# Optimization experiments

Measured on AMD Instinct MI355X. Metric: run time of the kernel, lower is better.

The kernel has to match this reference:

```python
import jax, jax.numpy as jnp
import numpy as np

D = 512      # d_model
H = 8        # n_heads
HD = D // H  # head_dim = 64
PS = 4       # patch_size
B, T, P = 4, 4096, 1024


def setup_inputs() -> dict:
    key = jax.random.key(0)
    ks = jax.random.split(key, 12)
    s = 1.0 / np.sqrt(D)
    return {
        "token_hidden": jax.random.normal(ks[0], (B, T, D), jnp.float32),
        "patch_hidden": jax.random.normal(ks[1], (B, P, D), jnp.float32),
        "Wq": jax.random.normal(ks[2], (D, D), jnp.float32) * s,
        "Wk": jax.random.normal(ks[3], (D, D), jnp.float32) * s,
        "Wv": jax.random.normal(ks[4], (D, D), jnp.float32) * s,
        "bq": jax.random.normal(ks[5], (D,), jnp.float32) * 0.02,
        "bk": jax.random.normal(ks[6], (D,), jnp.float32) * 0.02,
        "bv": jax.random.normal(ks[7], (D,), jnp.float32) * 0.02,
        "Wo": jax.random.normal(ks[8], (D, D), jnp.float32) * s,
        "bo": jax.random.normal(ks[9], (D,), jnp.float32) * 0.02,
    }


def reference(token_hidden, patch_hidden, Wq, Wk, Wv, bq, bk, bv, Wo, bo):
    b, t, _ = token_hidden.shape
    p = patch_hidden.shape[1]
    # QKV projections (equivalent to nn.MultiheadAttention in_proj)
    q = (token_hidden @ Wq + bq).reshape(b, t, H, HD)
    k = (patch_hidden @ Wk + bk).reshape(b, p, H, HD)
    v = (patch_hidden @ Wv + bv).reshape(b, p, H, HD)
    # scaled dot-product scores: [b, h, t, p]
    scores = jnp.einsum('bthd,bphd->bhtp', q, k) / jnp.sqrt(jnp.asarray(HD, q.dtype))
    # block-causal token-to-patch mask: token i attends to patches 0..i//PS
    allowed = jnp.arange(p)[None, :] <= (jnp.arange(t)[:, None] // PS)  # [t, p]
    scores = jnp.where(allowed[None, None, :, :], scores, -jnp.inf)
    attn = jax.nn.softmax(scores, axis=-1)
    ctx = jnp.einsum('bhtp,bphd->bthd', attn, v).reshape(b, t, D)
    out = ctx @ Wo + bo  # out_proj
    return token_hidden + out
```

## Files before the change

kernel.cpp:

```cpp
#include <hip/hip_runtime.h>
#include <stdint.h>

#define DM 512
#define NH 8
#define HDIM 64
#define TT 4096
#define PP 1024

typedef float f32x4 __attribute__((ext_vector_type(4)));
typedef __bf16 bf16x8 __attribute__((ext_vector_type(8)));
typedef unsigned short u16x8 __attribute__((ext_vector_type(8)));
typedef unsigned short u16x4 __attribute__((ext_vector_type(4)));
typedef unsigned int u32x2 __attribute__((ext_vector_type(2)));

static __device__ __forceinline__ unsigned short f2bf(float f) {
  unsigned u = __builtin_bit_cast(unsigned, f);
  u += 0x7fff + ((u >> 16) & 1);
  return (unsigned short)(u >> 16);
}

static __device__ __forceinline__ unsigned packbf(float a, float b) {
  unsigned ua = __builtin_bit_cast(unsigned, a) + 0x8000u;
  unsigned ub = __builtin_bit_cast(unsigned, b) + 0x8000u;
  return __builtin_amdgcn_perm(ub, ua, 0x07060302u);
}

static __device__ __forceinline__ void load_lds16(const void* g, void* l) {
  __builtin_amdgcn_global_load_lds(
      (__attribute__((address_space(1))) void*)g,
      (__attribute__((address_space(3))) void*)l, 16, 0, 0);
}

static __device__ __forceinline__ f32x4 mfma16(bf16x8 a, bf16x8 b, f32x4 c) {
  return __builtin_amdgcn_mfma_f32_16x16x32_bf16(a, b, c, 0, 0, 0);
}

__global__ __launch_bounds__(256) void k_convert(
    const float* __restrict__ tok, const float* __restrict__ pat,
    const float* __restrict__ wq, const float* __restrict__ wk,
    const float* __restrict__ wv, const float* __restrict__ wo,
    unsigned short* __restrict__ xtok, unsigned short* __restrict__ xpat,
    unsigned short* __restrict__ wt) {
  const int gid = blockIdx.x * 256 + threadIdx.x;
  const int NX = 2621440;
  if (gid < NX) {
    int i4 = gid * 4;
    const float* src;
    unsigned short* dst;
    int idx;
    if (i4 < 8388608) { src = tok; dst = xtok; idx = i4; }
    else              { src = pat; dst = xpat; idx = i4 - 8388608; }
    f32x4 v = *(const f32x4*)&src[idx];
    u16x4 o;
#pragma unroll
    for (int i = 0; i < 4; ++i) o[i] = f2bf(v[i]);
    *(u16x4*)&dst[idx] = o;
  } else {
    int wi = gid - NX;
    int wid = wi >> 16;
    int e = (wi & 65535) << 2;
    int k = e >> 9, n = e & 511;
    const float* w = (wid == 0) ? wq : (wid == 1) ? wk : (wid == 2) ? wv : wo;
    f32x4 v = *(const f32x4*)&w[e];
    unsigned short* wtb = wt + (wid << 18);
#pragma unroll
    for (int i = 0; i < 4; ++i) wtb[(n + i) * 512 + k] = f2bf(v[i]);
  }
}

__device__ __forceinline__ void gemm_body(
    const unsigned short* __restrict__ A, const unsigned short* __restrict__ Wt,
    const float* __restrict__ bias, unsigned short* __restrict__ outb,
    float* __restrict__ outf, const float* __restrict__ resid, int mode,
    int bid, unsigned short* sA, unsigned short* sB) {
  const int tid = threadIdx.x;
  const int wave = tid >> 6, lane = tid & 63;
  const int q = lane >> 4, c = lane & 15;
  const int bm = bid >> 2, bn = bid & 3;
  const int wm = (wave >> 1) * 64, wn = (wave & 1) * 64;
  const int lr = lane >> 2, lc = (lane & 3) * 8;

  f32x4 acc[4][4];
#pragma unroll
  for (int i = 0; i < 4; ++i)
#pragma unroll
    for (int j = 0; j < 4; ++j) acc[i][j] = (f32x4){0.f, 0.f, 0.f, 0.f};

  const int rowA0 = bm * 128, rowB0 = bn * 128;

  for (int k0 = 0; k0 < 512; k0 += 32) {
#pragma unroll
    for (int qq = 0; qq < 2; ++qq) {
      const int chunk = wave * 2 + qq;
      load_lds16(&A[(rowA0 + chunk * 16 + lr) * 512 + k0 + lc], &sA[chunk * 512]);
      load_lds16(&Wt[(rowB0 + chunk * 16 + lr) * 512 + k0 + lc], &sB[chunk * 512]);
    }
    __syncthreads();
    bf16x8 af[4], bfr[4];
#pragma unroll
    for (int mt = 0; mt < 4; ++mt)
      af[mt] = __builtin_bit_cast(bf16x8, *(const u16x8*)&sA[(wm + mt * 16 + c) * 32 + q * 8]);
#pragma unroll
    for (int nt = 0; nt < 4; ++nt)
      bfr[nt] = __builtin_bit_cast(bf16x8, *(const u16x8*)&sB[(wn + nt * 16 + c) * 32 + q * 8]);
#pragma unroll
    for (int mt = 0; mt < 4; ++mt)
#pragma unroll
      for (int nt = 0; nt < 4; ++nt)
        acc[mt][nt] = mfma16(af[mt], bfr[nt], acc[mt][nt]);
    __syncthreads();
  }

  const float vs = (mode == 0) ? 0.125f : 1.0f;
#pragma unroll
  for (int nt = 0; nt < 4; ++nt) {
    const int col = bn * 128 + wn + nt * 16 + c;
    const float bcol = bias[col];
#pragma unroll
    for (int mt = 0; mt < 4; ++mt) {
      const int row0 = bm * 128 + wm + mt * 16 + q * 4;
#pragma unroll
      for (int r = 0; r < 4; ++r) {
        const int row = row0 + r;
        const float v = (acc[mt][nt][r] + bcol) * vs;
        if (mode == 3) {
          const int o = row * 512 + col;
          outf[o] = v + resid[o];
        } else if (mode == 2) {
          outb[((row >> 10) << 19) + (col << 10) + (row & 1023)] = f2bf(v);
        } else {
          outb[row * 512 + col] = f2bf(v);
        }
      }
    }
  }
}

__global__ __launch_bounds__(256) void k_gemm(
    const unsigned short* __restrict__ A, const unsigned short* __restrict__ Wt,
    const float* __restrict__ bias, unsigned short* __restrict__ outb,
    float* __restrict__ outf, const float* __restrict__ resid, int mode) {
  __shared__ unsigned short sA[128 * 32];
  __shared__ unsigned short sB[128 * 32];
  gemm_body(A, Wt, bias, outb, outf, resid, mode, blockIdx.x, sA, sB);
}

__global__ __launch_bounds__(256) void k_gemm_kv(
    const unsigned short* __restrict__ A,
    const unsigned short* __restrict__ WtK, const unsigned short* __restrict__ WtV,
    const float* __restrict__ bk, const float* __restrict__ bv,
    unsigned short* __restrict__ KB, unsigned short* __restrict__ VTB) {
  __shared__ unsigned short sA[128 * 32];
  __shared__ unsigned short sB[128 * 32];
  const int kv = blockIdx.x >> 7;
  const int bid = blockIdx.x & 127;
  if (kv == 0)
    gemm_body(A, WtK, bk, KB, nullptr, nullptr, 1, bid, sA, sB);
  else
    gemm_body(A, WtV, bv, VTB, nullptr, nullptr, 2, bid, sA, sB);
}

__global__ __launch_bounds__(256) void k_attn(
    const unsigned short* __restrict__ Q,
    const unsigned short* __restrict__ K,
    const unsigned short* __restrict__ VT,
    unsigned short* __restrict__ CTX) {
  __shared__ unsigned short sK[32 * 80];
  __shared__ unsigned short sV[64 * 40];
  __shared__ unsigned short sPT[4 * 32 * 40];

  const int tid = threadIdx.x;
  const int lane = tid & 63;
  const int wave = tid >> 6;
  const int q = lane >> 4, c = lane & 15;

  const int i = blockIdx.x >> 5;
  const int tg = (i & 1) ? (31 - (i >> 1)) : (i >> 1);
  const int bh = blockIdx.x & 31;
  const int b = bh >> 3, h = bh & 7;
  const int t0 = tg * 128 + wave * 32;
  const int tA = t0 + c, tB = t0 + 16 + c;

  const int qbA = (b * TT + tA) * 512 + h * 64 + q * 8;
  const int qbB = (b * TT + tB) * 512 + h * 64 + q * 8;
  const bf16x8 qfA0 = __builtin_bit_cast(bf16x8, *(const u16x8*)&Q[qbA]);
  const bf16x8 qfA1 = __builtin_bit_cast(bf16x8, *(const u16x8*)&Q[qbA + 32]);
  const bf16x8 qfB0 = __builtin_bit_cast(bf16x8, *(const u16x8*)&Q[qbB]);
  const bf16x8 qfB1 = __builtin_bit_cast(bf16x8, *(const u16x8*)&Q[qbB + 32]);

  f32x4 oA[4], oB[4];
#pragma unroll
  for (int m = 0; m < 4; ++m) {
    oA[m] = (f32x4){0.f, 0.f, 0.f, 0.f};
    oB[m] = (f32x4){0.f, 0.f, 0.f, 0.f};
  }
  f32x4 lA = (f32x4){0.f, 0.f, 0.f, 0.f};
  f32x4 lB = lA;
  const u16x8 onesu = {0x3F80, 0x3F80, 0x3F80, 0x3F80, 0x3F80, 0x3F80, 0x3F80, 0x3F80};
  const bf16x8 ones = __builtin_bit_cast(bf16x8, onesu);

  const int ntile = tg + 1;
  const int krow = tid >> 3, kcol = (tid & 7) * 8;
  const int vrow = tid >> 2, vcol = (tid & 3) * 8;
  const int kg = (b * PP + krow) * 512 + h * 64 + kcol;
  const int vg = (b << 19) + ((h * 64 + vrow) << 10) + vcol;
  unsigned short* sp = &sPT[wave * 1280];

  for (int pt = 0; pt < ntile; ++pt) {
    const int p0 = pt * 32;
    const u16x8 kreg = *(const u16x8*)&K[kg + p0 * 512];
    const u16x8 vreg = *(const u16x8*)&VT[vg + p0];
    __syncthreads();
    *(u16x8*)&sK[krow * 80 + kcol] = kreg;
    *(u16x8*)&sV[vrow * 40 + vcol] = vreg;
    __syncthreads();

    const bf16x8 ka0 = __builtin_bit_cast(bf16x8, *(const u16x8*)&sK[c * 80 + q * 8]);
    const bf16x8 ka1 = __builtin_bit_cast(bf16x8, *(const u16x8*)&sK[c * 80 + 32 + q * 8]);
    const bf16x8 kb0 = __builtin_bit_cast(bf16x8, *(const u16x8*)&sK[(16 + c) * 80 + q * 8]);
    const bf16x8 kb1 = __builtin_bit_cast(bf16x8, *(const u16x8*)&sK[(16 + c) * 80 + 32 + q * 8]);

    const f32x4 z = (f32x4){0.f, 0.f, 0.f, 0.f};
    f32x4 sA0 = mfma16(ka1, qfA1, mfma16(ka0, qfA0, z));
    f32x4 sA1 = mfma16(kb1, qfA1, mfma16(kb0, qfA0, z));
    f32x4 sB0 = mfma16(ka1, qfB1, mfma16(ka0, qfB0, z));
    f32x4 sB1 = mfma16(kb1, qfB1, mfma16(kb0, qfB0, z));

    if (pt + 1 == ntile) {
      const int limA = tA >> 2, limB = tB >> 2;
      const int pb0 = p0 + q * 4, pb1 = p0 + 16 + q * 4;
#pragma unroll
      for (int r = 0; r < 4; ++r) {
        if (pb0 + r > limA) sA0[r] = -1e30f;
        if (pb1 + r > limA) sA1[r] = -1e30f;
        if (pb0 + r > limB) sB0[r] = -1e30f;
        if (pb1 + r > limB) sB1[r] = -1e30f;
      }
    }

    float pA0[4], pA1[4], pB0[4], pB1[4];
#pragma unroll
    for (int r = 0; r < 4; ++r) {
      pA0[r] = __expf(sA0[r]);
      pA1[r] = __expf(sA1[r]);
      pB0[r] = __expf(sB0[r]);
      pB1[r] = __expf(sB1[r]);
    }

    {
      u32x2 w;
      w[0] = packbf(pA0[0], pA0[1]); w[1] = packbf(pA0[2], pA0[3]);
      *(u32x2*)&sp[c * 40 + q * 4] = w;
      w[0] = packbf(pA1[0], pA1[1]); w[1] = packbf(pA1[2], pA1[3]);
      *(u32x2*)&sp[c * 40 + 16 + q * 4] = w;
      w[0] = packbf(pB0[0], pB0[1]); w[1] = packbf(pB0[2], pB0[3]);
      *(u32x2*)&sp[(16 + c) * 40 + q * 4] = w;
      w[0] = packbf(pB1[0], pB1[1]); w[1] = packbf(pB1[2], pB1[3]);
      *(u32x2*)&sp[(16 + c) * 40 + 16 + q * 4] = w;
    }
    const bf16x8 pbA = __builtin_bit_cast(bf16x8, *(const u16x8*)&sp[c * 40 + q * 8]);
    const bf16x8 pbB = __builtin_bit_cast(bf16x8, *(const u16x8*)&sp[(16 + c) * 40 + q * 8]);

#pragma unroll
    for (int mt = 0; mt < 4; ++mt) {
      const bf16x8 vf =
          __builtin_bit_cast(bf16x8, *(const u16x8*)&sV[(mt * 16 + c) * 40 + q * 8]);
      oA[mt] = mfma16(vf, pbA, oA[mt]);
      oB[mt] = mfma16(vf, pbB, oB[mt]);
    }
    lA = mfma16(ones, pbA, lA);
    lB = mfma16(ones, pbB, lB);
  }

  const float invA = 1.f / lA[0];
  const float invB = 1.f / lB[0];
  const int obA = (b * TT + tA) * 512 + h * 64 + q * 4;
  const int obB = (b * TT + tB) * 512 + h * 64 + q * 4;
#pragma unroll
  for (int mt = 0; mt < 4; ++mt) {
    u16x4 oa, ob;
#pragma unroll
    for (int r = 0; r < 4; ++r) {
      oa[r] = f2bf(oA[mt][r] * invA);
      ob[r] = f2bf(oB[mt][r] * invB);
    }
    *(u16x4*)&CTX[obA + mt * 16] = oa;
    *(u16x4*)&CTX[obB + mt * 16] = ob;
  }
}

extern "C" void kernel_launch(void* const* d_in, const int* in_sizes, int n_in,
                              void* d_out, int out_size, void* d_ws, size_t ws_size,
                              hipStream_t stream) {
  const float* tok = (const float*)d_in[0];
  const float* pat = (const float*)d_in[1];
  const float* Wq = (const float*)d_in[2];
  const float* Wk = (const float*)d_in[3];
  const float* Wv = (const float*)d_in[4];
  const float* bq = (const float*)d_in[5];
  const float* bk = (const float*)d_in[6];
  const float* bv = (const float*)d_in[7];
  const float* Wo = (const float*)d_in[8];
  const float* bo = (const float*)d_in[9];
  float* out = (float*)d_out;

  unsigned short* ws = (unsigned short*)d_ws;
  unsigned short* XTOK = ws;
  unsigned short* XPAT = ws + 8388608;
  unsigned short* WT = ws + 10485760;
  unsigned short* QB = ws + 11534336;
  unsigned short* KB = ws + 19922944;
  unsigned short* VTB = ws + 22020096;

  k_convert<<<11264, 256, 0, stream>>>(tok, pat, Wq, Wk, Wv, Wo, XTOK, XPAT, WT);
  k_gemm<<<512, 256, 0, stream>>>(XTOK, WT, bq, QB, nullptr, nullptr, 0);
  k_gemm_kv<<<256, 256, 0, stream>>>(XPAT, WT + 262144, WT + 524288, bk, bv, KB, VTB);
  k_attn<<<1024, 256, 0, stream>>>(QB, KB, VTB, XTOK);
  k_gemm<<<512, 256, 0, stream>>>(XTOK, WT + 786432, bo, nullptr, out, tok, 3);
}
```

Measured before the change: 227.3 us.

## Fuse fp32-to-bf16 activation conversion into QKV GEMMs and double-buffer attention K/V

Removes the separate activation conversion pass: the QKV GEMM now reads fp32 token and patch activations directly, packs them to bf16 into padded LDS, and runs Q, K and V in a single launch. Q is prescaled by log2(e)/8 so attention can use a native exp2. P is packed to bf16 by truncation instead of rounding. Attention K/V tiles are double-buffered in LDS with register prefetch, cutting one barrier per tile. The cost is more fp32 global traffic and VALU work inside the GEMM loads, plus slightly lower precision in the packed probabilities.

```diff
diff --git a/kernel.cpp b/kernel.cpp
--- a/kernel.cpp
+++ b/kernel.cpp
@@ -12,6 +12,7 @@
 typedef unsigned short u16x8 __attribute__((ext_vector_type(8)));
 typedef unsigned short u16x4 __attribute__((ext_vector_type(4)));
 typedef unsigned int u32x2 __attribute__((ext_vector_type(2)));
+typedef unsigned int u32x4 __attribute__((ext_vector_type(4)));
 
 static __device__ __forceinline__ unsigned short f2bf(float f) {
   unsigned u = __builtin_bit_cast(unsigned, f);
@@ -19,10 +20,22 @@
   return (unsigned short)(u >> 16);
 }
 
-static __device__ __forceinline__ unsigned packbf(float a, float b) {
+static __device__ __forceinline__ unsigned packrnd(float a, float b) {
   unsigned ua = __builtin_bit_cast(unsigned, a) + 0x8000u;
   unsigned ub = __builtin_bit_cast(unsigned, b) + 0x8000u;
   return __builtin_amdgcn_perm(ub, ua, 0x07060302u);
+}
+static __device__ __forceinline__ unsigned packtr(float a, float b) {
+  return __builtin_amdgcn_perm(__builtin_bit_cast(unsigned, b),
+                               __builtin_bit_cast(unsigned, a), 0x07060302u);
+}
+
+static __device__ __forceinline__ float fexp2(float x) {
+#if __has_builtin(__builtin_amdgcn_exp2f)
+  return __builtin_amdgcn_exp2f(x);
+#else
+  return __expf(x * 0.69314718055994531f);
+#endif
 }
 
 static __device__ __forceinline__ void load_lds16(const void* g, void* l) {
@@ -35,44 +48,26 @@
   return __builtin_amdgcn_mfma_f32_16x16x32_bf16(a, b, c, 0, 0, 0);
 }
 
-__global__ __launch_bounds__(256) void k_convert(
-    const float* __restrict__ tok, const float* __restrict__ pat,
+__global__ __launch_bounds__(256) void k_wconv(
     const float* __restrict__ wq, const float* __restrict__ wk,
     const float* __restrict__ wv, const float* __restrict__ wo,
-    unsigned short* __restrict__ xtok, unsigned short* __restrict__ xpat,
     unsigned short* __restrict__ wt) {
-  const int gid = blockIdx.x * 256 + threadIdx.x;
-  const int NX = 2621440;
-  if (gid < NX) {
-    int i4 = gid * 4;
-    const float* src;
-    unsigned short* dst;
-    int idx;
-    if (i4 < 8388608) { src = tok; dst = xtok; idx = i4; }
-    else              { src = pat; dst = xpat; idx = i4 - 8388608; }
-    f32x4 v = *(const f32x4*)&src[idx];
-    u16x4 o;
-#pragma unroll
-    for (int i = 0; i < 4; ++i) o[i] = f2bf(v[i]);
-    *(u16x4*)&dst[idx] = o;
-  } else {
-    int wi = gid - NX;
-    int wid = wi >> 16;
-    int e = (wi & 65535) << 2;
-    int k = e >> 9, n = e & 511;
-    const float* w = (wid == 0) ? wq : (wid == 1) ? wk : (wid == 2) ? wv : wo;
-    f32x4 v = *(const f32x4*)&w[e];
-    unsigned short* wtb = wt + (wid << 18);
-#pragma unroll
-    for (int i = 0; i < 4; ++i) wtb[(n + i) * 512 + k] = f2bf(v[i]);
-  }
-}
-
-__device__ __forceinline__ void gemm_body(
-    const unsigned short* __restrict__ A, const unsigned short* __restrict__ Wt,
+  const int wi = blockIdx.x * 256 + threadIdx.x;
+  const int wid = wi >> 16;
+  const int e = (wi & 65535) << 2;
+  const int k = e >> 9, n = e & 511;
+  const float* w = (wid == 0) ? wq : (wid == 1) ? wk : (wid == 2) ? wv : wo;
+  f32x4 v = *(const f32x4*)&w[e];
+  unsigned short* wtb = wt + (wid << 18);
+#pragma unroll
+  for (int i = 0; i < 4; ++i) wtb[(n + i) * 512 + k] = f2bf(v[i]);
+}
+
+template <int MODE>
+__device__ __forceinline__ void gemm_fp32_body(
+    const float* __restrict__ A, const unsigned short* __restrict__ Wt,
     const float* __restrict__ bias, unsigned short* __restrict__ outb,
-    float* __restrict__ outf, const float* __restrict__ resid, int mode,
-    int bid, unsigned short* sA, unsigned short* sB) {
+    int bid, unsigned short* sA, unsigned short* sB, float scale) {
   const int tid = threadIdx.x;
   const int wave = tid >> 6, lane = tid & 63;
   const int q = lane >> 4, c = lane & 15;
@@ -92,14 +87,22 @@
 #pragma unroll
     for (int qq = 0; qq < 2; ++qq) {
       const int chunk = wave * 2 + qq;
-      load_lds16(&A[(rowA0 + chunk * 16 + lr) * 512 + k0 + lc], &sA[chunk * 512]);
-      load_lds16(&Wt[(rowB0 + chunk * 16 + lr) * 512 + k0 + lc], &sB[chunk * 512]);
+      const int row = chunk * 16 + lr;
+      load_lds16(&Wt[(rowB0 + row) * 512 + k0 + lc], &sB[chunk * 512]);
+      const f32x4 a0 = *(const f32x4*)&A[(rowA0 + row) * 512 + k0 + lc];
+      const f32x4 a1 = *(const f32x4*)&A[(rowA0 + row) * 512 + k0 + lc + 4];
+      u32x4 pk;
+      pk[0] = packrnd(a0[0], a0[1]);
+      pk[1] = packrnd(a0[2], a0[3]);
+      pk[2] = packrnd(a1[0], a1[1]);
+      pk[3] = packrnd(a1[2], a1[3]);
+      *(u32x4*)&sA[row * 40 + lc] = pk;
     }
     __syncthreads();
     bf16x8 af[4], bfr[4];
 #pragma unroll
     for (int mt = 0; mt < 4; ++mt)
-      af[mt] = __builtin_bit_cast(bf16x8, *(const u16x8*)&sA[(wm + mt * 16 + c) * 32 + q * 8]);
+      af[mt] = __builtin_bit_cast(bf16x8, *(const u16x8*)&sA[(wm + mt * 16 + c) * 40 + q * 8]);
 #pragma unroll
     for (int nt = 0; nt < 4; ++nt)
       bfr[nt] = __builtin_bit_cast(bf16x8, *(const u16x8*)&sB[(wn + nt * 16 + c) * 32 + q * 8]);
@@ -111,7 +114,6 @@
     __syncthreads();
   }
 
-  const float vs = (mode == 0) ? 0.125f : 1.0f;
 #pragma unroll
   for (int nt = 0; nt < 4; ++nt) {
     const int col = bn * 128 + wn + nt * 16 + c;
@@ -122,11 +124,8 @@
 #pragma unroll
       for (int r = 0; r < 4; ++r) {
         const int row = row0 + r;
-        const float v = (acc[mt][nt][r] + bcol) * vs;
-        if (mode == 3) {
-          const int o = row * 512 + col;
-          outf[o] = v + resid[o];
-        } else if (mode == 2) {
+        const float v = (acc[mt][nt][r] + bcol) * scale;
+        if (MODE == 2) {
           outb[((row >> 10) << 19) + (col << 10) + (row & 1023)] = f2bf(v);
         } else {
           outb[row * 512 + col] = f2bf(v);
@@ -136,28 +135,84 @@
   }
 }
 
-__global__ __launch_bounds__(256) void k_gemm(
+__global__ __launch_bounds__(256) void k_gemm_qkv(
+    const float* __restrict__ tok, const float* __restrict__ pat,
+    const unsigned short* __restrict__ WT,
+    const float* __restrict__ bq, const float* __restrict__ bk,
+    const float* __restrict__ bv,
+    unsigned short* __restrict__ QB, unsigned short* __restrict__ KB,
+    unsigned short* __restrict__ VTB) {
+  __shared__ unsigned short sA[128 * 40];
+  __shared__ unsigned short sB[128 * 32];
+  const int bid = blockIdx.x;
+  if (bid < 512) {
+    gemm_fp32_body<0>(tok, WT, bq, QB, bid, sA, sB, 0.18033688011112042f);
+  } else if (bid < 640) {
+    gemm_fp32_body<1>(pat, WT + 262144, bk, KB, bid - 512, sA, sB, 1.0f);
+  } else {
+    gemm_fp32_body<2>(pat, WT + 524288, bv, VTB, bid - 640, sA, sB, 1.0f);
+  }
+}
+
+__global__ __launch_bounds__(256) void k_gemm_o(
     const unsigned short* __restrict__ A, const unsigned short* __restrict__ Wt,
-    const float* __restrict__ bias, unsigned short* __restrict__ outb,
-    float* __restrict__ outf, const float* __restrict__ resid, int mode) {
+    const float* __restrict__ bias, float* __restrict__ outf,
+    const float* __restrict__ resid) {
   __shared__ unsigned short sA[128 * 32];
   __shared__ unsigned short sB[128 * 32];
-  gemm_body(A, Wt, bias, outb, outf, resid, mode, blockIdx.x, sA, sB);
-}
-
-__global__ __launch_bounds__(256) void k_gemm_kv(
-    const unsigned short* __restrict__ A,
-    const unsigned short* __restrict__ WtK, const unsigned short* __restrict__ WtV,
-    const float* __restrict__ bk, const float* __restrict__ bv,
-    unsigned short* __restrict__ KB, unsigned short* __restrict__ VTB) {
-  __shared__ unsigned short sA[128 * 32];
-  __shared__ unsigned short sB[128 * 32];
-  const int kv = blockIdx.x >> 7;
-  const int bid = blockIdx.x & 127;
-  if (kv == 0)
-    gemm_body(A, WtK, bk, KB, nullptr, nullptr, 1, bid, sA, sB);
-  else
-    gemm_body(A, WtV, bv, VTB, nullptr, nullptr, 2, bid, sA, sB);
+  const int tid = threadIdx.x;
+  const int wave = tid >> 6, lane = tid & 63;
+  const int q = lane >> 4, c = lane & 15;
+  const int bm = blockIdx.x >> 2, bn = blockIdx.x & 3;
+  const int wm = (wave >> 1) * 64, wn = (wave & 1) * 64;
+  const int lr = lane >> 2, lc = (lane & 3) * 8;
+
+  f32x4 acc[4][4];
+#pragma unroll
+  for (int i = 0; i < 4; ++i)
+#pragma unroll
+    for (int j = 0; j < 4; ++j) acc[i][j] = (f32x4){0.f, 0.f, 0.f, 0.f};
+
+  const int rowA0 = bm * 128, rowB0 = bn * 128;
+
+  for (int k0 = 0; k0 < 512; k0 += 32) {
+#pragma unroll
+    for (int qq = 0; qq < 2; ++qq) {
+      const int chunk = wave * 2 + qq;
+      load_lds16(&A[(rowA0 + chunk * 16 + lr) * 512 + k0 + lc], &sA[chunk * 512]);
+      load_lds16(&Wt[(rowB0 + chunk * 16 + lr) * 512 + k0 + lc], &sB[chunk * 512]);
+    }
+    __syncthreads();
+    bf16x8 af[4], bfr[4];
+#pragma unroll
+    for (int mt = 0; mt < 4; ++mt)
+      af[mt] = __builtin_bit_cast(bf16x8, *(const u16x8*)&sA[(wm + mt * 16 + c) * 32 + q * 8]);
+#pragma unroll
+    for (int nt = 0; nt < 4; ++nt)
+      bfr[nt] = __builtin_bit_cast(bf16x8, *(const u16x8*)&sB[(wn + nt * 16 + c) * 32 + q * 8]);
+#pragma unroll
+    for (int mt = 0; mt < 4; ++mt)
+#pragma unroll
+      for (int nt = 0; nt < 4; ++nt)
+        acc[mt][nt] = mfma16(af[mt], bfr[nt], acc[mt][nt]);
+    __syncthreads();
+  }
+
+#pragma unroll
+  for (int nt = 0; nt < 4; ++nt) {
+    const int col = bn * 128 + wn + nt * 16 + c;
+    const float bcol = bias[col];
+#pragma unroll
+    for (int mt = 0; mt < 4; ++mt) {
+      const int row0 = bm * 128 + wm + mt * 16 + q * 4;
+#pragma unroll
+      for (int r = 0; r < 4; ++r) {
+        const int row = row0 + r;
+        const int o = row * 512 + col;
+        outf[o] = acc[mt][nt][r] + bcol + resid[o];
+      }
+    }
+  }
 }
 
 __global__ __launch_bounds__(256) void k_attn(
@@ -165,9 +220,9 @@
     const unsigned short* __restrict__ K,
     const unsigned short* __restrict__ VT,
     unsigned short* __restrict__ CTX) {
-  __shared__ unsigned short sK[32 * 80];
-  __shared__ unsigned short sV[64 * 40];
-  __shared__ unsigned short sPT[4 * 32 * 40];
+  __shared__ unsigned short sK[2][32 * 88];
+  __shared__ unsigned short sV[2][64 * 40];
+  __shared__ unsigned short sPT[4][32 * 40];
 
   const int tid = threadIdx.x;
   const int lane = tid & 63;
@@ -204,21 +259,28 @@
   const int vrow = tid >> 2, vcol = (tid & 3) * 8;
   const int kg = (b * PP + krow) * 512 + h * 64 + kcol;
   const int vg = (b << 19) + ((h * 64 + vrow) << 10) + vcol;
-  unsigned short* sp = &sPT[wave * 1280];
+  unsigned short* sp = sPT[wave];
+
+  u16x8 kreg = *(const u16x8*)&K[kg];
+  u16x8 vreg = *(const u16x8*)&VT[vg];
+  *(u16x8*)&sK[0][krow * 88 + kcol] = kreg;
+  *(u16x8*)&sV[0][vrow * 40 + vcol] = vreg;
+  __syncthreads();
 
   for (int pt = 0; pt < ntile; ++pt) {
-    const int p0 = pt * 32;
-    const u16x8 kreg = *(const u16x8*)&K[kg + p0 * 512];
-    const u16x8 vreg = *(const u16x8*)&VT[vg + p0];
-    __syncthreads();
-    *(u16x8*)&sK[krow * 80 + kcol] = kreg;
-    *(u16x8*)&sV[vrow * 40 + vcol] = vreg;
-    __syncthreads();
-
-    const bf16x8 ka0 = __builtin_bit_cast(bf16x8, *(const u16x8*)&sK[c * 80 + q * 8]);
-    const bf16x8 ka1 = __builtin_bit_cast(bf16x8, *(const u16x8*)&sK[c * 80 + 32 + q * 8]);
-    const bf16x8 kb0 = __builtin_bit_cast(bf16x8, *(const u16x8*)&sK[(16 + c) * 80 + q * 8]);
-    const bf16x8 kb1 = __builtin_bit_cast(bf16x8, *(const u16x8*)&sK[(16 + c) * 80 + 32 + q * 8]);
+    const int buf = pt & 1;
+    const bool more = (pt + 1 < ntile);
+    if (more) {
+      kreg = *(const u16x8*)&K[kg + (pt + 1) * 32 * 512];
+      vreg = *(const u16x8*)&VT[vg + (pt + 1) * 32];
+    }
+    const unsigned short* bK = sK[buf];
+    const unsigned short* bV = sV[buf];
+
+    const bf16x8 ka0 = __builtin_bit_cast(bf16x8, *(const u16x8*)&bK[c * 88 + q * 8]);
+    const bf16x8 ka1 = __builtin_bit_cast(bf16x8, *(const u16x8*)&bK[c * 88 + 32 + q * 8]);
+    const bf16x8 kb0 = __builtin_bit_cast(bf16x8, *(const u16x8*)&bK[(16 + c) * 88 + q * 8]);
+    const bf16x8 kb1 = __builtin_bit_cast(bf16x8, *(const u16x8*)&bK[(16 + c) * 88 + 32 + q * 8]);
 
     const f32x4 z = (f32x4){0.f, 0.f, 0.f, 0.f};
     f32x4 sA0 = mfma16(ka1, qfA1, mfma16(ka0, qfA0, z));
@@ -227,6 +289,7 @@
     f32x4 sB1 = mfma16(kb1, qfB1, mfma16(kb0, qfB0, z));
 
     if (pt + 1 == ntile) {
+      const int p0 = pt * 32;
       const int limA = tA >> 2, limB = tB >> 2;
       const int pb0 = p0 + q * 4, pb1 = p0 + 16 + q * 4;
 #pragma unroll
@@ -241,21 +304,21 @@
     float pA0[4], pA1[4], pB0[4], pB1[4];
 #pragma unroll
     for (int r = 0; r < 4; ++r) {
-      pA0[r] = __expf(sA0[r]);
-      pA1[r] = __expf(sA1[r]);
-      pB0[r] = __expf(sB0[r]);
-      pB1[r] = __expf(sB1[r]);
+      pA0[r] = fexp2(sA0[r]);
+      pA1[r] = fexp2(sA1[r]);
+      pB0[r] = fexp2(sB0[r]);
+      pB1[r] = fexp2(sB1[r]);
     }
 
     {
       u32x2 w;
-      w[0] = packbf(pA0[0], pA0[1]); w[1] = packbf(pA0[2], pA0[3]);
+      w[0] = packtr(pA0[0], pA0[1]); w[1] = packtr(pA0[2], pA0[3]);
       *(u32x2*)&sp[c * 40 + q * 4] = w;
-      w[0] = packbf(pA1[0], pA1[1]); w[1] = packbf(pA1[2], pA1[3]);
+      w[0] = packtr(pA1[0], pA1[1]); w[1] = packtr(pA1[2], pA1[3]);
       *(u32x2*)&sp[c * 40 + 16 + q * 4] = w;
-      w[0] = packbf(pB0[0], pB0[1]); w[1] = packbf(pB0[2], pB0[3]);
+      w[0] = packtr(pB0[0], pB0[1]); w[1] = packtr(pB0[2], pB0[3]);
       *(u32x2*)&sp[(16 + c) * 40 + q * 4] = w;
-      w[0] = packbf(pB1[0], pB1[1]); w[1] = packbf(pB1[2], pB1[3]);
+      w[0] = packtr(pB1[0], pB1[1]); w[1] = packtr(pB1[2], pB1[3]);
       *(u32x2*)&sp[(16 + c) * 40 + 16 + q * 4] = w;
     }
     const bf16x8 pbA = __builtin_bit_cast(bf16x8, *(const u16x8*)&sp[c * 40 + q * 8]);
@@ -264,12 +327,18 @@
 #pragma unroll
     for (int mt = 0; mt < 4; ++mt) {
       const bf16x8 vf =
-          __builtin_bit_cast(bf16x8, *(const u16x8*)&sV[(mt * 16 + c) * 40 + q * 8]);
+          __builtin_bit_cast(bf16x8, *(const u16x8*)&bV[(mt * 16 + c) * 40 + q * 8]);
       oA[mt] = mfma16(vf, pbA, oA[mt]);
       oB[mt] = mfma16(vf, pbB, oB[mt]);
     }
     lA = mfma16(ones, pbA, lA);
     lB = mfma16(ones, pbB, lB);
+
+    if (more) {
+      *(u16x8*)&sK[buf ^ 1][krow * 88 + kcol] = kreg;
+      *(u16x8*)&sV[buf ^ 1][vrow * 40 + vcol] = vreg;
+      __syncthreads();
+    }
   }
 
   const float invA = 1.f / lA[0];
@@ -305,16 +374,14 @@
   float* out = (float*)d_out;
 
   unsigned short* ws = (unsigned short*)d_ws;
-  unsigned short* XTOK = ws;
-  unsigned short* XPAT = ws + 8388608;
-  unsigned short* WT = ws + 10485760;
-  unsigned short* QB = ws + 11534336;
-  unsigned short* KB = ws + 19922944;
-  unsigned short* VTB = ws + 22020096;
-
-  k_convert<<<11264, 256, 0, stream>>>(tok, pat, Wq, Wk, Wv, Wo, XTOK, XPAT, WT);
-  k_gemm<<<512, 256, 0, stream>>>(XTOK, WT, bq, QB, nullptr, nullptr, 0);
-  k_gemm_kv<<<256, 256, 0, stream>>>(XPAT, WT + 262144, WT + 524288, bk, bv, KB, VTB);
-  k_attn<<<1024, 256, 0, stream>>>(QB, KB, VTB, XTOK);
-  k_gemm<<<512, 256, 0, stream>>>(XTOK, WT + 786432, bo, nullptr, out, tok, 3);
-}
+  unsigned short* WT = ws;
+  unsigned short* QB = ws + 2097152;
+  unsigned short* KB = ws + 10485760;
+  unsigned short* VTB = ws + 12582912;
+  unsigned short* CTX = ws + 14680064;
+
+  k_wconv<<<1024, 256, 0, stream>>>(Wq, Wk, Wv, Wo, WT);
+  k_gemm_qkv<<<768, 256, 0, stream>>>(tok, pat, WT, bq, bk, bv, QB, KB, VTB);
+  k_attn<<<1024, 256, 0, stream>>>(QB, KB, VTB, CTX);
+  k_gemm_o<<<512, 256, 0, stream>>>(CTX, WT + 786432, bo, out, tok);
+}
```

After: 203.0 us. -10.7%, faster.
